# Optimization experiments

Measured on AMD Instinct MI355X. Metric: run time of the kernel, lower is better.

## Reference

```python
import jax, jax.numpy as jnp
import numpy as np

B = 4096
IN = 1024   # complex input size (real tensor width = 2*IN)
H = 1024    # complex hidden size
G = 4       # gates: f, i, a, o


def _cproj(xr, xi, Wr, Wi, br, bi):
    # Complex linear over a stacked gate axis.
    # xr, xi: [B, D]; Wr, Wi: [G, H, D]; br, bi: [G, H] -> ([B,G,H], [B,G,H])
    zr = jnp.einsum('bd,god->bgo', xr, Wr) - jnp.einsum('bd,god->bgo', xi, Wi) + br
    zi = jnp.einsum('bd,god->bgo', xr, Wi) + jnp.einsum('bd,god->bgo', xi, Wr) + bi
    return zr, zi


def _ctimes(ar, ai, br, bi):
    # complex elementwise multiply (a_r + i a_i) * (b_r + i b_i)
    return ar * br - ai * bi, ar * bi + ai * br


def setup_inputs() -> dict:
    key = jax.random.key(0)
    ks = jax.random.split(key, 11)
    s_in = 1.0 / np.sqrt(2 * IN)
    s_h = 1.0 / np.sqrt(2 * H)
    return {
        'input': jax.random.normal(ks[0], (B, 2 * IN), jnp.float32),
        'h_x': jax.random.normal(ks[1], (B, 2 * H), jnp.float32),
        'c_x': jax.random.normal(ks[2], (B, 2 * H), jnp.float32),
        # input-side CLinear weights stacked over gates [f, i, a, o]
        'Uw_r': jax.random.normal(ks[3], (G, H, IN), jnp.float32) * s_in,
        'Uw_i': jax.random.normal(ks[4], (G, H, IN), jnp.float32) * s_in,
        'Ub_r': jax.random.normal(ks[5], (G, H), jnp.float32) * s_in,
        'Ub_i': jax.random.normal(ks[6], (G, H), jnp.float32) * s_in,
        # hidden-side CLinear weights stacked over gates [f, i, a, o]
        'Ww_r': jax.random.normal(ks[7], (G, H, H), jnp.float32) * s_h,
        'Ww_i': jax.random.normal(ks[8], (G, H, H), jnp.float32) * s_h,
        'Wb_r': jax.random.normal(ks[9], (G, H), jnp.float32) * s_h,
        'Wb_i': jax.random.normal(ks[10], (G, H), jnp.float32) * s_h,
    }


def reference(input, h_x, c_x, Uw_r, Uw_i, Ub_r, Ub_i, Ww_r, Ww_i, Wb_r, Wb_i):
    xr, xi = input[:, :IN], input[:, IN:]
    hr, hi = h_x[:, :H], h_x[:, H:]
    cr, ci = c_x[:, :H], c_x[:, H:]

    # fused gate projections: z = W(h) + U(x), complex-valued, [B, 4, H]
    zu_r, zu_i = _cproj(xr, xi, Uw_r, Uw_i, Ub_r, Ub_i)
    zh_r, zh_i = _cproj(hr, hi, Ww_r, Ww_i, Wb_r, Wb_i)
    zr = zu_r + zh_r
    zi = zu_i + zh_i

    # gate activations (applied elementwise to real and imag halves alike)
    fr, fi = jax.nn.sigmoid(zr[:, 0]), jax.nn.sigmoid(zi[:, 0])
    ir, ii = jax.nn.sigmoid(zr[:, 1]), jax.nn.sigmoid(zi[:, 1])
    ar, ai = jnp.tanh(zr[:, 2]), jnp.tanh(zi[:, 2])
    orr, oi = jax.nn.sigmoid(zr[:, 3]), jax.nn.sigmoid(zi[:, 3])

    cf_r, cf_i = _ctimes(cr, ci, fr, fi)
    ai_r, ai_i = _ctimes(ar, ai, ir, ii)
    ct_r, ct_i = cf_r + ai_r, cf_i + ai_i

    ht_r, ht_i = _ctimes(orr, oi, jnp.tanh(ct_r), jnp.tanh(ct_i))

    h_t = jnp.concatenate((ht_r, ht_i), axis=1)
    c_t = jnp.concatenate((ct_r, ct_i), axis=1)
    return h_t, c_t
```

## Files before the change

kernel.cpp:

```cpp
#include <hip/hip_runtime.h>
#include <cstddef>


typedef short bf16x8 __attribute__((ext_vector_type(8)));
typedef float f32x4  __attribute__((ext_vector_type(4)));
typedef unsigned int u32x4 __attribute__((ext_vector_type(4)));

static constexpr int KDIM = 4096;
static constexpr size_t HOFF = (size_t)4096 * 2048;

__device__ __forceinline__ unsigned short f2bf(float f) {
    unsigned u = __float_as_uint(f);
    u += 0x7FFF + ((u >> 16) & 1);
    return (unsigned short)(u >> 16);
}

__device__ __forceinline__ u32x4 pack8(float4 a, float4 b) {
    u32x4 v;
    v.x = (unsigned)f2bf(a.x) | ((unsigned)f2bf(a.y) << 16);
    v.y = (unsigned)f2bf(a.z) | ((unsigned)f2bf(a.w) << 16);
    v.z = (unsigned)f2bf(b.x) | ((unsigned)f2bf(b.y) << 16);
    v.w = (unsigned)f2bf(b.z) | ((unsigned)f2bf(b.w) << 16);
    return v;
}

__device__ __forceinline__ float4 neg4(float4 v) {
    return make_float4(-v.x, -v.y, -v.z, -v.w);
}

__device__ __forceinline__ void async16(const void* g, void* l) {
    __builtin_amdgcn_global_load_lds(
        (const __attribute__((address_space(1))) unsigned int*)g,
        (__attribute__((address_space(3))) unsigned int*)l,
        16, 0, 0);
}

__device__ __forceinline__ float sigm(float x) { return 1.0f / (1.0f + __expf(-x)); }
__device__ __forceinline__ float tanh_(float x) {
    float e = __expf(2.0f * x);
    return (e - 1.0f) / (e + 1.0f);
}

__global__ __launch_bounds__(256) void pack_all(
    const float* __restrict__ input, const float* __restrict__ hx,
    const float* __restrict__ Uw_r, const float* __restrict__ Uw_i,
    const float* __restrict__ Ww_r, const float* __restrict__ Ww_i,
    const float* __restrict__ Ub_r, const float* __restrict__ Ub_i,
    const float* __restrict__ Wb_r, const float* __restrict__ Wb_i,
    unsigned short* __restrict__ Xb, unsigned short* __restrict__ Wb16,
    float* __restrict__ biasp) {
    int bid = blockIdx.x;
    if (bid < 8192) {
        int idx = bid * 256 + threadIdx.x;
        int r    = idx >> 9;
        int gcol = (idx & 511) * 8;
        const float* src = (gcol < 2048) ? (input + (size_t)r * 2048 + gcol)
                                         : (hx    + (size_t)r * 2048 + (gcol - 2048));
        float4 f0 = *(const float4*)src;
        float4 f1 = *(const float4*)(src + 4);
        *(u32x4*)(Xb + (size_t)idx * 8) = pack8(f0, f1);
    } else {
        int idx = (bid - 8192) * 256 + threadIdx.x;
        int np = idx >> 9;
        int c8 = idx & 511;
        int k  = c8 * 8;
        int o = np >> 2, g = np & 3;
        int q = k >> 10, d = k & 1023;
        size_t sidx = (size_t)g * (1024 * 1024) + (size_t)o * 1024 + d;
        const float* srcR = (q < 2 ? Uw_r : Ww_r) + sidx;
        const float* srcI = (q < 2 ? Uw_i : Ww_i) + sidx;
        float4 r0 = *(const float4*)srcR; float4 r1 = *(const float4*)(srcR + 4);
        float4 i0 = *(const float4*)srcI; float4 i1 = *(const float4*)(srcI + 4);
        int n0 = o * 8 + g * 2;
        u32x4 p0, p1;
        if (q & 1) { p0 = pack8(neg4(i0), neg4(i1)); p1 = pack8(r0, r1); }
        else       { p0 = pack8(r0, r1);             p1 = pack8(i0, i1); }
        *(u32x4*)(Wb16 + (size_t)n0 * KDIM + k)       = p0;
        *(u32x4*)(Wb16 + (size_t)(n0 + 1) * KDIM + k) = p1;
        if (c8 == 0) {
            size_t bi = (size_t)g * 1024 + o;
            biasp[n0]     = Ub_r[bi] + Wb_r[bi];
            biasp[n0 + 1] = Ub_i[bi] + Wb_i[bi];
        }
    }
}

__global__ __launch_bounds__(256) void clstm_gemm(
    const unsigned short* __restrict__ Xb,
    const unsigned short* __restrict__ Wb,
    const float* __restrict__ biasp,
    const float* __restrict__ c_x,
    float* __restrict__ out) {
    __shared__ __align__(16) char smem[32768];
    char* sA = smem;
    char* sB = smem + 16384;

    const int tid  = threadIdx.x;
    const int lane = tid & 63;
    const int wave = tid >> 6;
    const int wm = wave >> 1, wn = wave & 1;
    const int quad = lane >> 4, col16 = lane & 15;

    const int bid = blockIdx.x;
    const int st = bid >> 5;
    const int wi = bid & 31;
    const int mblock = (st & 7) * 4 + (wi & 3);
    const int nblock = (st >> 3) * 8 + (wi >> 2);

    const int rbase = tid >> 3;
    const int csw   = (tid & 7) ^ (rbase & 7);
    const unsigned short* pa[4];
    const unsigned short* pb[4];
#pragma unroll
    for (int i = 0; i < 4; ++i) {
        pa[i] = Xb + (size_t)(mblock * 128 + i * 32 + rbase) * KDIM + csw * 8;
        pb[i] = Wb + (size_t)(nblock * 128 + i * 32 + rbase) * KDIM + csw * 8;
    }

    f32x4 acc[4][4] = {};

    for (int kt = 0; kt < 64; ++kt) {
        __syncthreads();
#pragma unroll
        for (int i = 0; i < 4; ++i) {
            async16(pa[i], sA + i * 4096 + wave * 1024);
            async16(pb[i], sB + i * 4096 + wave * 1024);
            pa[i] += 64; pb[i] += 64;
        }
        __syncthreads();
#pragma unroll
        for (int s = 0; s < 2; ++s) {
            bf16x8 af[4], bf[4];
#pragma unroll
            for (int t = 0; t < 4; ++t) {
                int mr = wm * 64 + t * 16 + col16;
                int ch = (s * 4 + quad) ^ (mr & 7);
                af[t] = *(const bf16x8*)(sA + mr * 128 + ch * 16);
                int nr = wn * 64 + t * 16 + col16;
                int ch2 = (s * 4 + quad) ^ (nr & 7);
                bf[t] = *(const bf16x8*)(sB + nr * 128 + ch2 * 16);
            }
#pragma unroll
            for (int tm = 0; tm < 4; ++tm)
#pragma unroll
                for (int tn = 0; tn < 4; ++tn)
                    acc[tm][tn] = __builtin_amdgcn_mfma_f32_16x16x32_bf16(
                        af[tm], bf[tn], acc[tm][tn], 0, 0, 0);
        }
    }

    __syncthreads();
    float* zs = (float*)(smem + wave * 8192);
    const float* bp = biasp + nblock * 128 + wn * 64;
    const int o_idx = lane & 3;
    const int rgrp  = lane >> 2;

    for (int p = 0; p < 4; ++p) {
        const int h   = p >> 1;
        const int seg = p & 1;
#pragma unroll
        for (int tm2 = 0; tm2 < 2; ++tm2)
#pragma unroll
            for (int tl = 0; tl < 2; ++tl) {
                int tn = h * 2 + tl;
                int colz = tl * 16 + col16;
#pragma unroll
                for (int r = 0; r < 4; ++r)
                    zs[(tm2 * 16 + quad * 4 + r) * 40 + colz] = acc[seg * 2 + tm2][tn][r];
            }

        float4 bb0 = *(const float4*)(bp + h * 32 + o_idx * 8);
        float4 bb1 = *(const float4*)(bp + h * 32 + o_idx * 8 + 4);
        int o_glob = nblock * 16 + wn * 8 + h * 4 + o_idx;

#pragma unroll
        for (int t = 0; t < 2; ++t) {
            int rowz = rgrp + t * 16;
            const float* zp = zs + rowz * 40 + o_idx * 8;
            float4 z0 = *(const float4*)zp;
            float4 z1 = *(const float4*)(zp + 4);
            int b = mblock * 128 + wm * 64 + seg * 32 + rowz;

            float fr = sigm(z0.x + bb0.x), fi = sigm(z0.y + bb0.y);
            float ir = sigm(z0.z + bb0.z), ii = sigm(z0.w + bb0.w);
            float ar = tanh_(z1.x + bb1.x), ai = tanh_(z1.y + bb1.y);
            float og_r = sigm(z1.z + bb1.z), og_i = sigm(z1.w + bb1.w);

            float cr = c_x[(size_t)b * 2048 + o_glob];
            float ci = c_x[(size_t)b * 2048 + 1024 + o_glob];

            float ct_r = (cr * fr - ci * fi) + (ar * ir - ai * ii);
            float ct_i = (cr * fi + ci * fr) + (ar * ii + ai * ir);
            float tr = tanh_(ct_r), ti = tanh_(ct_i);
            float ht_r = og_r * tr - og_i * ti;
            float ht_i = og_r * ti + og_i * tr;

            out[(size_t)b * 2048 + o_glob]               = ht_r;
            out[(size_t)b * 2048 + 1024 + o_glob]        = ht_i;
            out[HOFF + (size_t)b * 2048 + o_glob]        = ct_r;
            out[HOFF + (size_t)b * 2048 + 1024 + o_glob] = ct_i;
        }
        if (p < 3) __builtin_amdgcn_s_waitcnt(0);
    }
}

extern "C" void kernel_launch(void* const* d_in, const int* in_sizes, int n_in,
                              void* d_out, int out_size, void* d_ws, size_t ws_size,
                              hipStream_t stream) {
    const float* input = (const float*)d_in[0];
    const float* h_x   = (const float*)d_in[1];
    const float* c_x   = (const float*)d_in[2];
    const float* Uw_r  = (const float*)d_in[3];
    const float* Uw_i  = (const float*)d_in[4];
    const float* Ub_r  = (const float*)d_in[5];
    const float* Ub_i  = (const float*)d_in[6];
    const float* Ww_r  = (const float*)d_in[7];
    const float* Ww_i  = (const float*)d_in[8];
    const float* Wb_r  = (const float*)d_in[9];
    const float* Wb_i  = (const float*)d_in[10];
    float* out = (float*)d_out;

    unsigned short* Xb   = (unsigned short*)d_ws;
    unsigned short* Wb16 = Xb + (size_t)4096 * 4096;
    float* biasp = (float*)(Wb16 + (size_t)8192 * 4096);

    pack_all<<<16384, 256, 0, stream>>>(input, h_x, Uw_r, Uw_i, Ww_r, Ww_i,
                                        Ub_r, Ub_i, Wb_r, Wb_i, Xb, Wb16, biasp);
    clstm_gemm<<<2048, 256, 0, stream>>>(Xb, Wb16, biasp, c_x, out);
}
```

Measured before the change: 484.3 us.

## Use 256x256 tiles with 8 waves and double-buffered async LDS loads

The GEMM tile grows from 128x128 to 256x256 with 512 threads (8 waves, each computing 128x64), and the LDS tiles are double-buffered so the next K-slab loads asynchronously while MFMAs run on the current one. Block-ID swizzling changes the order tiles are assigned across the grid, and s_setprio around the MFMA clusters is meant to favour math issue. The aim is more data reuse per LDS load and hiding global load latency. The cost is 128KB of dynamic LDS and larger accumulator register pressure, which limits occupancy, and the epilogue loop grows to eight passes. The occupancy hint in the launch bounds (2 blocks) is unlikely to be reachable with that much LDS.

```diff
diff --git a/kernel.cpp b/kernel.cpp
--- a/kernel.cpp
+++ b/kernel.cpp
@@ -85,93 +85,130 @@
     }
 }
 
-__global__ __launch_bounds__(256) void clstm_gemm(
+__global__ __launch_bounds__(512, 2) void clstm_gemm(
     const unsigned short* __restrict__ Xb,
     const unsigned short* __restrict__ Wb,
     const float* __restrict__ biasp,
     const float* __restrict__ c_x,
     float* __restrict__ out) {
-    __shared__ __align__(16) char smem[32768];
-    char* sA = smem;
-    char* sB = smem + 16384;
+    extern __shared__ char smem[];
 
     const int tid  = threadIdx.x;
     const int lane = tid & 63;
     const int wave = tid >> 6;
-    const int wm = wave >> 1, wn = wave & 1;
+    const int wm = wave >> 2, wn = wave & 3;
     const int quad = lane >> 4, col16 = lane & 15;
 
     const int bid = blockIdx.x;
-    const int st = bid >> 5;
-    const int wi = bid & 31;
-    const int mblock = (st & 7) * 4 + (wi & 3);
-    const int nblock = (st >> 3) * 8 + (wi >> 2);
-
-    const int rbase = tid >> 3;
-    const int csw   = (tid & 7) ^ (rbase & 7);
+    const int swz = (bid & 7) * 64 + (bid >> 3);
+    const int st = swz >> 5, wi = swz & 31;
+    const int mtile = (st & 3) * 4 + (wi & 3);
+    const int ntile = (st >> 2) * 8 + (wi >> 2);
+
+    const int srow  = tid >> 3;
+    const int sslot = tid & 7;
     const unsigned short* pa[4];
     const unsigned short* pb[4];
 #pragma unroll
     for (int i = 0; i < 4; ++i) {
-        pa[i] = Xb + (size_t)(mblock * 128 + i * 32 + rbase) * KDIM + csw * 8;
-        pb[i] = Wb + (size_t)(nblock * 128 + i * 32 + rbase) * KDIM + csw * 8;
-    }
-
-    f32x4 acc[4][4] = {};
-
+        const int rowA = i * 64 + srow;
+        const int c = sslot ^ (rowA & 7);
+        pa[i] = Xb + (size_t)(mtile * 256 + rowA) * KDIM + c * 8;
+        pb[i] = Wb + (size_t)(ntile * 256 + rowA) * KDIM + c * 8;
+    }
+
+    f32x4 acc[8][4] = {};
+
+#pragma unroll
+    for (int i = 0; i < 4; ++i) {
+        async16(pa[i], smem + i * 8192 + wave * 1024);
+        async16(pb[i], smem + 32768 + i * 8192 + wave * 1024);
+        pa[i] += 64; pb[i] += 64;
+    }
+
+    const int rA0 = wm * 128 + col16;
+    const int rB0 = wn * 64 + col16;
+
+#pragma unroll 2
     for (int kt = 0; kt < 64; ++kt) {
-        __syncthreads();
-#pragma unroll
-        for (int i = 0; i < 4; ++i) {
-            async16(pa[i], sA + i * 4096 + wave * 1024);
-            async16(pb[i], sB + i * 4096 + wave * 1024);
-            pa[i] += 64; pb[i] += 64;
-        }
-        __syncthreads();
-#pragma unroll
-        for (int s = 0; s < 2; ++s) {
-            bf16x8 af[4], bf[4];
-#pragma unroll
-            for (int t = 0; t < 4; ++t) {
-                int mr = wm * 64 + t * 16 + col16;
-                int ch = (s * 4 + quad) ^ (mr & 7);
-                af[t] = *(const bf16x8*)(sA + mr * 128 + ch * 16);
-                int nr = wn * 64 + t * 16 + col16;
-                int ch2 = (s * 4 + quad) ^ (nr & 7);
-                bf[t] = *(const bf16x8*)(sB + nr * 128 + ch2 * 16);
+        char* sA  = smem + (kt & 1) * 65536;
+        char* sB  = sA + 32768;
+        char* sAn = smem + (((kt & 1) ^ 1)) * 65536;
+        char* sBn = sAn + 32768;
+
+        if (kt < 63) {
+#pragma unroll
+            for (int i = 0; i < 4; ++i) {
+                async16(pa[i], sAn + i * 8192 + wave * 1024);
+                async16(pb[i], sBn + i * 8192 + wave * 1024);
+                pa[i] += 64; pb[i] += 64;
             }
-#pragma unroll
-            for (int tm = 0; tm < 4; ++tm)
-#pragma unroll
-                for (int tn = 0; tn < 4; ++tn)
-                    acc[tm][tn] = __builtin_amdgcn_mfma_f32_16x16x32_bf16(
-                        af[tm], bf[tn], acc[tm][tn], 0, 0, 0);
+            asm volatile("s_waitcnt vmcnt(8)" ::: "memory");
+        } else {
+            asm volatile("s_waitcnt vmcnt(0)" ::: "memory");
+        }
+        __builtin_amdgcn_s_barrier();
+
+        bf16x8 bfr[4][2];
+#pragma unroll
+        for (int n = 0; n < 4; ++n)
+#pragma unroll
+            for (int ks = 0; ks < 2; ++ks) {
+                const int r = rB0 + n * 16;
+                const int ch = (ks * 4 + quad) ^ (r & 7);
+                bfr[n][ks] = *(const bf16x8*)(sB + r * 128 + ch * 16);
+            }
+
+#pragma unroll
+        for (int p = 0; p < 4; ++p) {
+            bf16x8 af[2][2];
+#pragma unroll
+            for (int f = 0; f < 2; ++f)
+#pragma unroll
+                for (int ks = 0; ks < 2; ++ks) {
+                    const int r = rA0 + p * 32 + f * 16;
+                    const int ch = (ks * 4 + quad) ^ (r & 7);
+                    af[f][ks] = *(const bf16x8*)(sA + r * 128 + ch * 16);
+                }
+            __builtin_amdgcn_s_barrier();
+            __builtin_amdgcn_s_setprio(1);
+#pragma unroll
+            for (int f = 0; f < 2; ++f)
+#pragma unroll
+                for (int n = 0; n < 4; ++n) {
+                    acc[p * 2 + f][n] = __builtin_amdgcn_mfma_f32_16x16x32_bf16(
+                        af[f][0], bfr[n][0], acc[p * 2 + f][n], 0, 0, 0);
+                    acc[p * 2 + f][n] = __builtin_amdgcn_mfma_f32_16x16x32_bf16(
+                        af[f][1], bfr[n][1], acc[p * 2 + f][n], 0, 0, 0);
+                }
+            __builtin_amdgcn_s_setprio(0);
+            __builtin_amdgcn_s_barrier();
         }
     }
 
     __syncthreads();
     float* zs = (float*)(smem + wave * 8192);
-    const float* bp = biasp + nblock * 128 + wn * 64;
+    const float* bp = biasp + ntile * 256 + wn * 64;
     const int o_idx = lane & 3;
     const int rgrp  = lane >> 2;
 
-    for (int p = 0; p < 4; ++p) {
-        const int h   = p >> 1;
-        const int seg = p & 1;
-#pragma unroll
-        for (int tm2 = 0; tm2 < 2; ++tm2)
+    for (int pass = 0; pass < 8; ++pass) {
+        const int seg = pass >> 1;
+        const int h   = pass & 1;
+#pragma unroll
+        for (int mf2 = 0; mf2 < 2; ++mf2)
 #pragma unroll
             for (int tl = 0; tl < 2; ++tl) {
-                int tn = h * 2 + tl;
+                int nf = h * 2 + tl;
                 int colz = tl * 16 + col16;
 #pragma unroll
                 for (int r = 0; r < 4; ++r)
-                    zs[(tm2 * 16 + quad * 4 + r) * 40 + colz] = acc[seg * 2 + tm2][tn][r];
+                    zs[(mf2 * 16 + quad * 4 + r) * 40 + colz] = acc[seg * 2 + mf2][nf][r];
             }
 
         float4 bb0 = *(const float4*)(bp + h * 32 + o_idx * 8);
         float4 bb1 = *(const float4*)(bp + h * 32 + o_idx * 8 + 4);
-        int o_glob = nblock * 16 + wn * 8 + h * 4 + o_idx;
+        int o_glob = ntile * 32 + wn * 8 + h * 4 + o_idx;
 
 #pragma unroll
         for (int t = 0; t < 2; ++t) {
@@ -179,7 +216,7 @@
             const float* zp = zs + rowz * 40 + o_idx * 8;
             float4 z0 = *(const float4*)zp;
             float4 z1 = *(const float4*)(zp + 4);
-            int b = mblock * 128 + wm * 64 + seg * 32 + rowz;
+            int b = mtile * 256 + wm * 128 + seg * 32 + rowz;
 
             float fr = sigm(z0.x + bb0.x), fi = sigm(z0.y + bb0.y);
             float ir = sigm(z0.z + bb0.z), ii = sigm(z0.w + bb0.w);
@@ -200,7 +237,7 @@
             out[HOFF + (size_t)b * 2048 + o_glob]        = ct_r;
             out[HOFF + (size_t)b * 2048 + 1024 + o_glob] = ct_i;
         }
-        if (p < 3) __builtin_amdgcn_s_waitcnt(0);
+        if (pass < 7) __builtin_amdgcn_s_waitcnt(0);
     }
 }
 
@@ -224,7 +261,14 @@
     unsigned short* Wb16 = Xb + (size_t)4096 * 4096;
     float* biasp = (float*)(Wb16 + (size_t)8192 * 4096);
 
+    static bool s_attr = false;
+    if (!s_attr) {
+        hipFuncSetAttribute((const void*)clstm_gemm,
+                            hipFuncAttributeMaxDynamicSharedMemorySize, 131072);
+        s_attr = true;
+    }
+
     pack_all<<<16384, 256, 0, stream>>>(input, h_x, Uw_r, Uw_i, Ww_r, Ww_i,
                                         Ub_r, Ub_i, Wb_r, Wb_i, Xb, Wb16, biasp);
-    clstm_gemm<<<2048, 256, 0, stream>>>(Xb, Wb16, biasp, c_x, out);
-}
+    clstm_gemm<<<512, 512, 131072, stream>>>(Xb, Wb16, biasp, c_x, out);
+}
```

New measurement: 557.0 us. 1.15x slower.
